# Kernel tuning notes

Hardware: AMD Instinct MI355X
Metric: run time of the kernel (lower is better)

## Reference

```python
import jax, jax.numpy as jnp
import numpy as np

EPS = 1e-6
NUM_HEADS = 16

def layernorm(x, alpha, bias):
    # Faithful to the torch module: torch.std uses ddof=1, and eps is added to std.
    mean = jnp.mean(x, axis=-1, keepdims=True)
    std = jnp.std(x, axis=-1, keepdims=True, ddof=1)
    return alpha * (x - mean) / (std + EPS) + bias

def setup_inputs() -> dict:
    key = jax.random.key(0)
    B, S, D, F = 4, 2048, 1024, 4096
    ks = jax.random.split(key, 8)
    s = 1.0 / np.sqrt(D)
    inp = {
        'x': jax.random.normal(ks[0], (B, S, D), jnp.float32),
        'src_mask': jnp.ones((B, 1, 1, S), jnp.int32),
        'wq': jax.random.normal(ks[1], (D, D), jnp.float32) * s,
        'bq': jnp.zeros((D,), jnp.float32),
        'wk': jax.random.normal(ks[2], (D, D), jnp.float32) * s,
        'bk': jnp.zeros((D,), jnp.float32),
        'wv': jax.random.normal(ks[3], (D, D), jnp.float32) * s,
        'bv': jnp.zeros((D,), jnp.float32),
        'wo': jax.random.normal(ks[4], (D, D), jnp.float32) * s,
        'bo': jnp.zeros((D,), jnp.float32),
        'w1': jax.random.normal(ks[5], (D, F), jnp.float32) * s,
        'b1': jnp.zeros((F,), jnp.float32),
        'w2': jax.random.normal(ks[6], (F, D), jnp.float32) * (1.0 / np.sqrt(F)),
        'b2': jnp.zeros((D,), jnp.float32),
        'ln1_a': jnp.ones((D,), jnp.float32),
        'ln1_b': jnp.zeros((D,), jnp.float32),
        'ln2_a': jnp.ones((D,), jnp.float32),
        'ln2_b': jnp.zeros((D,), jnp.float32),
    }
    return inp

def mha(x, src_mask, wq, bq, wk, bk, wv, bv, wo, bo):
    B, S, D = x.shape
    H = NUM_HEADS
    dk = D // H
    q = (x @ wq + bq).reshape(B, S, H, dk).transpose(0, 2, 1, 3)  # [B,H,S,dk]
    k = (x @ wk + bk).reshape(B, S, H, dk).transpose(0, 2, 1, 3)
    v = (x @ wv + bv).reshape(B, S, H, dk).transpose(0, 2, 1, 3)
    scores = jnp.einsum('bhqd,bhkd->bhqk', q, k) / np.sqrt(dk)  # [B,H,S,S]
    scores = jnp.where(src_mask == 0, -1e9, scores)
    p = jax.nn.softmax(scores, axis=-1)
    ctx = jnp.einsum('bhqk,bhkd->bhqd', p, v)  # [B,H,S,dk]
    ctx = ctx.transpose(0, 2, 1, 3).reshape(B, S, D)
    return ctx @ wo + bo

def reference(x, src_mask, wq, bq, wk, bk, wv, bv, wo, bo,
              w1, b1, w2, b2, ln1_a, ln1_b, ln2_a, ln2_b):
    # residual 1: pre-norm self-attention (dropout is identity in eval)
    h = x + mha(layernorm(x, ln1_a, ln1_b), src_mask, wq, bq, wk, bk, wv, bv, wo, bo)
    # residual 2: pre-norm FFN
    hn = layernorm(h, ln2_a, ln2_b)
    ffn = jax.nn.relu(hn @ w1 + b1) @ w2 + b2
    return h + ffn
```

## Files before the change

### kernel.cpp

```cpp
#include <hip/hip_runtime.h>
#include <hip/hip_bf16.h>

typedef __attribute__((ext_vector_type(8))) short bf16x8;
typedef __attribute__((ext_vector_type(4))) float f32x4;
typedef __hip_bfloat16 bf16;
typedef unsigned short u16;

#define B_ 4
#define S_ 2048
#define D_ 1024
#define F_ 4096
#define H_ 16
#define MROWS 8192

__device__ __forceinline__ u16 f2bf_bits(float f){
  union{bf16 h; u16 u;} x; x.h = __float2bfloat16(f); return x.u;
}
__device__ __forceinline__ unsigned packbf(float a, float b){
  return (unsigned)f2bf_bits(a) | ((unsigned)f2bf_bits(b)<<16);
}
__device__ __forceinline__ void gll16(const bf16* gp, u16* lp){
  __builtin_amdgcn_global_load_lds(
      (const __attribute__((address_space(1))) void*)gp,
      (__attribute__((address_space(3))) void*)lp, 16, 0, 0);
}

__global__ __launch_bounds__(256) void transpose_to_bf16(
    const float* __restrict__ W, bf16* __restrict__ WT, int K, int N)
{
  __shared__ float t[32][33];
  int n0 = blockIdx.x*32, k0 = blockIdx.y*32;
  int x = threadIdx.x, y = threadIdx.y;
  #pragma unroll
  for (int i=0;i<32;i+=8)
    t[y+i][x] = W[(size_t)(k0+y+i)*N + n0+x];
  __syncthreads();
  #pragma unroll
  for (int i=0;i<32;i+=8)
    WT[(size_t)(n0+y+i)*K + k0+x] = __float2bfloat16(t[x][y+i]);
}

__global__ __launch_bounds__(256) void concat_bias(
    const float* __restrict__ bq, const float* __restrict__ bk,
    const float* __restrict__ bv, float* __restrict__ out)
{
  int i = blockIdx.x*256 + threadIdx.x;
  float v = (i < 1024) ? bq[i] : (i < 2048) ? bk[i-1024] : bv[i-2048];
  out[i] = v;
}

__global__ __launch_bounds__(256) void v_transpose(
    const bf16* __restrict__ qkv, bf16* __restrict__ vT)
{
  __shared__ u16 tile[64*65];
  const int bh = blockIdx.y, b = bh>>4, h = bh&15;
  const int s0 = blockIdx.x*64;
  const int tid = threadIdx.x;
  const bf16* src = qkv + (size_t)(b*S_ + s0)*3072 + 2048 + h*64;
  #pragma unroll
  for (int i=0;i<2;i++){
    int idx = i*256 + tid;
    int r = idx>>3, sg = idx&7;
    uint4 v = *reinterpret_cast<const uint4*>(src + (size_t)r*3072 + sg*8);
    const u16* e = (const u16*)&v;
    #pragma unroll
    for (int j=0;j<8;j++) tile[r*65 + sg*8 + j] = e[j];
  }
  __syncthreads();
  bf16* dst = vT + (size_t)bh*64*S_ + s0;
  #pragma unroll
  for (int i=0;i<2;i++){
    int idx = i*256 + tid;
    int d = idx>>3, sg = idx&7;
    u16 tmp[8];
    #pragma unroll
    for (int j=0;j<8;j++) tmp[j] = tile[(sg*8+j)*65 + d];
    *reinterpret_cast<uint4*>(dst + (size_t)d*S_ + sg*8) = *reinterpret_cast<uint4*>(tmp);
  }
}

__device__ __forceinline__ float block_reduce_256(float v, float* sbuf){
  #pragma unroll
  for (int o=32;o>0;o>>=1) v += __shfl_down(v, o);
  int wave = threadIdx.x>>6;
  if ((threadIdx.x&63)==0) sbuf[wave] = v;
  __syncthreads();
  float r = sbuf[0]+sbuf[1]+sbuf[2]+sbuf[3];
  __syncthreads();
  return r;
}

__global__ __launch_bounds__(256) void ln_fwd(
    const float* __restrict__ x, const float* __restrict__ alpha,
    const float* __restrict__ beta, bf16* __restrict__ out)
{
  __shared__ float sbuf[4];
  int row = blockIdx.x, tid = threadIdx.x;
  const float4* xr = reinterpret_cast<const float4*>(x + (size_t)row*D_);
  float4 v = xr[tid];
  float sum = block_reduce_256(v.x+v.y+v.z+v.w, sbuf);
  float mean = sum * (1.0f/1024.0f);
  float dx0=v.x-mean, dx1=v.y-mean, dx2=v.z-mean, dx3=v.w-mean;
  float ssq = block_reduce_256(dx0*dx0+dx1*dx1+dx2*dx2+dx3*dx3, sbuf);
  float std_ = sqrtf(ssq * (1.0f/1023.0f));
  float inv = 1.0f/(std_ + 1e-6f);
  const float4* ar = reinterpret_cast<const float4*>(alpha);
  const float4* br = reinterpret_cast<const float4*>(beta);
  float4 a = ar[tid], bb = br[tid];
  unsigned* o = reinterpret_cast<unsigned*>(out + (size_t)row*D_);
  o[tid*2+0] = packbf(a.x*dx0*inv + bb.x, a.y*dx1*inv + bb.y);
  o[tid*2+1] = packbf(a.z*dx2*inv + bb.z, a.w*dx3*inv + bb.w);
}

template<int EPI>
__global__ __launch_bounds__(256) void gemm_bt(
    const bf16* __restrict__ A, const bf16* __restrict__ BT,
    const float* __restrict__ bias, const float* __restrict__ res,
    void* __restrict__ out, int M, int N, int K)
{
  __shared__ __align__(16) u16 As[128*32];
  __shared__ __align__(16) u16 Bs[128*32];
  const int tid = threadIdx.x;
  const int m0 = blockIdx.x*128, n0 = blockIdx.y*128;
  const int wave = tid>>6, lane = tid&63;
  const int wm = (wave>>1)*64, wn = (wave&1)*64;
  const int lrow = lane&15, quad = lane>>4;
  const int srow = wave*32 + (lane>>2);
  const int sseg = lane&3;
  const bf16* apg = A  + (size_t)(m0+srow)*K + sseg*8;
  const bf16* bpg = BT + (size_t)(n0+srow)*K + sseg*8;
  u16* asd = &As[wave*1024];
  u16* bsd = &Bs[wave*1024];

  f32x4 acc[4][4];
  #pragma unroll
  for (int i=0;i<4;i++)
    #pragma unroll
    for (int j=0;j<4;j++) acc[i][j] = (f32x4){0.f,0.f,0.f,0.f};

  for (int k0=0; k0<K; k0+=32) {
    gll16(apg + k0,                 asd);
    gll16(apg + k0 + (size_t)16*K,  asd + 512);
    gll16(bpg + k0,                 bsd);
    gll16(bpg + k0 + (size_t)16*K,  bsd + 512);
    __syncthreads();
    bf16x8 a[4], b[4];
    #pragma unroll
    for (int t=0;t<4;t++){
      a[t] = *reinterpret_cast<const bf16x8*>(&As[(wm + t*16 + lrow)*32 + quad*8]);
      b[t] = *reinterpret_cast<const bf16x8*>(&Bs[(wn + t*16 + lrow)*32 + quad*8]);
    }
    #pragma unroll
    for (int mt=0;mt<4;mt++)
      #pragma unroll
      for (int nt=0;nt<4;nt++)
        acc[mt][nt] = __builtin_amdgcn_mfma_f32_16x16x32_bf16(a[mt], b[nt], acc[mt][nt], 0,0,0);
    __syncthreads();
  }

  #pragma unroll
  for (int mt=0;mt<4;mt++){
    #pragma unroll
    for (int nt=0;nt<4;nt++){
      int col = n0 + wn + nt*16 + lrow;
      float bv = bias[col];
      #pragma unroll
      for (int r=0;r<4;r++){
        int row = m0 + wm + mt*16 + quad*4 + r;
        size_t idx = (size_t)row*N + col;
        float val = acc[mt][nt][r] + bv;
        if (EPI == 1) val = fmaxf(val, 0.0f);
        if (EPI == 2) {
          ((float*)out)[idx] = val + res[idx];
        } else {
          ((bf16*)out)[idx] = __float2bfloat16(val);
        }
      }
    }
  }
}

#define KP 72

__global__ __launch_bounds__(256) void flash_attn_mfma(
    const bf16* __restrict__ qkv, const bf16* __restrict__ vT,
    const int* __restrict__ mask, bf16* __restrict__ ctx)
{
  __shared__ __align__(16) u16 Ks[64*KP];
  __shared__ __align__(16) u16 Vt[64*KP];
  __shared__ __align__(16) u16 Ps[4][32*KP];
  __shared__ float Mb[64];

  const int b = blockIdx.z, h = blockIdx.y, qt = blockIdx.x;
  const int tid = threadIdx.x, wave = tid>>6, lane = tid&63;
  const int lr = lane&15, quad = lane>>4;
  const int qbase = qt*128 + wave*32;

  const bf16* base = qkv + (size_t)b*S_*3072 + h*64;
  const bf16* vtb  = vT + (size_t)(b*H_+h)*64*S_;
  const int*  mrow = mask + b*S_;

  bf16x8 qf[2][2];
  #pragma unroll
  for (int c=0;c<2;c++){
    const bf16* qp = base + (size_t)(qbase + c*16 + lr)*3072 + quad*8;
    qf[c][0] = *reinterpret_cast<const bf16x8*>(qp);
    qf[c][1] = *reinterpret_cast<const bf16x8*>(qp + 32);
  }

  f32x4 actx[2][4];
  #pragma unroll
  for (int c=0;c<2;c++)
    #pragma unroll
    for (int dt=0;dt<4;dt++) actx[c][dt] = (f32x4){0.f,0.f,0.f,0.f};
  float lsum[2][4] = {{0.f,0.f,0.f,0.f},{0.f,0.f,0.f,0.f}};

  u16* pw = &Ps[wave][0];

  for (int kt=0; kt<S_; kt+=64){
    #pragma unroll
    for (int i=0;i<2;i++){
      int idx = i*256 + tid;
      int r = idx>>3, sg = idx&7;
      *reinterpret_cast<uint4*>(&Ks[r*KP + sg*8]) =
        *reinterpret_cast<const uint4*>(base + 1024 + (size_t)(kt+r)*3072 + sg*8);
      *reinterpret_cast<uint4*>(&Vt[r*KP + sg*8]) =
        *reinterpret_cast<const uint4*>(vtb + (size_t)r*S_ + kt + sg*8);
    }
    if (tid < 64) Mb[tid] = (mrow[kt+tid]==0) ? -1e9f : 0.0f;
    __syncthreads();

    float p[2][4][4];
    #pragma unroll
    for (int nt=0;nt<4;nt++){
      bf16x8 kf0 = *reinterpret_cast<const bf16x8*>(&Ks[(nt*16+lr)*KP + quad*8]);
      bf16x8 kf1 = *reinterpret_cast<const bf16x8*>(&Ks[(nt*16+lr)*KP + 32 + quad*8]);
      float mb = Mb[nt*16+lr];
      #pragma unroll
      for (int c=0;c<2;c++){
        f32x4 a = (f32x4){0.f,0.f,0.f,0.f};
        a = __builtin_amdgcn_mfma_f32_16x16x32_bf16(qf[c][0], kf0, a, 0,0,0);
        a = __builtin_amdgcn_mfma_f32_16x16x32_bf16(qf[c][1], kf1, a, 0,0,0);
        #pragma unroll
        for (int r=0;r<4;r++){
          float e = __expf(a[r]*0.125f + mb);
          p[c][nt][r] = e;
          lsum[c][r] += e;
        }
      }
    }
    #pragma unroll
    for (int c=0;c<2;c++)
      #pragma unroll
      for (int nt=0;nt<4;nt++)
        #pragma unroll
        for (int r=0;r<4;r++)
          pw[(c*16+quad*4+r)*KP + nt*16 + lr] = f2bf_bits(p[c][nt][r]);

    bf16x8 pa[2][2];
    #pragma unroll
    for (int c=0;c<2;c++){
      pa[c][0] = *reinterpret_cast<const bf16x8*>(&pw[(c*16+lr)*KP + quad*8]);
      pa[c][1] = *reinterpret_cast<const bf16x8*>(&pw[(c*16+lr)*KP + 32 + quad*8]);
    }
    #pragma unroll
    for (int dt=0;dt<4;dt++){
      bf16x8 vf0 = *reinterpret_cast<const bf16x8*>(&Vt[(dt*16+lr)*KP + quad*8]);
      bf16x8 vf1 = *reinterpret_cast<const bf16x8*>(&Vt[(dt*16+lr)*KP + 32 + quad*8]);
      #pragma unroll
      for (int c=0;c<2;c++){
        actx[c][dt] = __builtin_amdgcn_mfma_f32_16x16x32_bf16(pa[c][0], vf0, actx[c][dt], 0,0,0);
        actx[c][dt] = __builtin_amdgcn_mfma_f32_16x16x32_bf16(pa[c][1], vf1, actx[c][dt], 0,0,0);
      }
    }
    __syncthreads();
  }

  #pragma unroll
  for (int c=0;c<2;c++)
    #pragma unroll
    for (int r=0;r<4;r++){
      float l = lsum[c][r];
      #pragma unroll
      for (int o=1;o<16;o<<=1) l += __shfl_xor(l, o);
      float inv = 1.0f/l;
      bf16* op = ctx + ((size_t)(b*S_ + qbase + c*16 + quad*4 + r))*D_ + h*64 + lr;
      #pragma unroll
      for (int dt=0;dt<4;dt++)
        op[dt*16] = __float2bfloat16(actx[c][dt][r]*inv);
    }
}

extern "C" void kernel_launch(void* const* d_in, const int* in_sizes, int n_in,
                              void* d_out, int out_size, void* d_ws, size_t ws_size,
                              hipStream_t stream) {
  const float* x    = (const float*)d_in[0];
  const int*   mask = (const int*)  d_in[1];
  const float* wq   = (const float*)d_in[2];
  const float* bq   = (const float*)d_in[3];
  const float* wk   = (const float*)d_in[4];
  const float* bk   = (const float*)d_in[5];
  const float* wv   = (const float*)d_in[6];
  const float* bv   = (const float*)d_in[7];
  const float* wo   = (const float*)d_in[8];
  const float* bo   = (const float*)d_in[9];
  const float* w1   = (const float*)d_in[10];
  const float* b1   = (const float*)d_in[11];
  const float* w2   = (const float*)d_in[12];
  const float* b2   = (const float*)d_in[13];
  const float* ln1a = (const float*)d_in[14];
  const float* ln1b = (const float*)d_in[15];
  const float* ln2a = (const float*)d_in[16];
  const float* ln2b = (const float*)d_in[17];

  char* ws = (char*)d_ws;
  bf16*  wqkvT = (bf16*) (ws + 0);
  bf16*  woT   = (bf16*) (ws + 6291456);
  bf16*  w1T   = (bf16*) (ws + 8388608);
  bf16*  w2T   = (bf16*) (ws + 16777216);
  float* bqkv  = (float*)(ws + 25165824);
  bf16*  xn    = (bf16*) (ws + 25178112);
  bf16*  vT    = (bf16*) (ws + 25178112);
  bf16*  qkv   = (bf16*) (ws + 41955328);
  bf16*  ctx   = (bf16*) (ws + 92286976);
  bf16*  hn    = (bf16*) (ws + 109064192);
  bf16*  act   = (bf16*) (ws + 25178112);

  dim3 tb(32,8);
  transpose_to_bf16<<<dim3(32,32), tb,0,stream>>>(wq, wqkvT,               1024,1024);
  transpose_to_bf16<<<dim3(32,32), tb,0,stream>>>(wk, wqkvT + 1024*1024,   1024,1024);
  transpose_to_bf16<<<dim3(32,32), tb,0,stream>>>(wv, wqkvT + 2*1024*1024, 1024,1024);
  transpose_to_bf16<<<dim3(32,32), tb,0,stream>>>(wo, woT,                 1024,1024);
  transpose_to_bf16<<<dim3(128,32),tb,0,stream>>>(w1, w1T,                 1024,4096);
  transpose_to_bf16<<<dim3(32,128),tb,0,stream>>>(w2, w2T,                 4096,1024);
  concat_bias<<<12,256,0,stream>>>(bq,bk,bv,bqkv);

  ln_fwd<<<8192,256,0,stream>>>(x, ln1a, ln1b, xn);
  gemm_bt<0><<<dim3(64,24),256,0,stream>>>(xn, wqkvT, bqkv, nullptr, qkv, MROWS,3072,1024);
  v_transpose<<<dim3(32,64),256,0,stream>>>(qkv, vT);
  flash_attn_mfma<<<dim3(S_/128,H_,B_),256,0,stream>>>(qkv, vT, mask, ctx);
  gemm_bt<2><<<dim3(64,8),256,0,stream>>>(ctx, woT, bo, x, d_out, MROWS,1024,1024);
  ln_fwd<<<8192,256,0,stream>>>((const float*)d_out, ln2a, ln2b, hn);
  gemm_bt<1><<<dim3(64,32),256,0,stream>>>(hn, w1T, b1, nullptr, act, MROWS,F_,1024);
  gemm_bt<2><<<dim3(64,8),256,0,stream>>>(act, w2T, b2, (const float*)d_out, d_out, MROWS,1024,F_);
}
```

Before: 607.9 us.

## Keep attention probabilities in registers via transposed MFMA and double queries per wave

The attention kernel now computes S^T (K as the A operand), so each lane's exp outputs already sit in the B-operand layout of a 16x16x16 bf16 MFMA for P·V. This removes the LDS round-trip for P, the per-wave Ps buffer and its writes and reads. Each wave now handles 64 query rows instead of 32, so each K/V tile is reused across twice as many queries, and the grid is halved. It also switches to exp2 with a folded scale, vectorized mask reads and packed output stores. The cost is higher register pressure from the larger accumulators and fewer blocks in flight.

```diff
diff --git a/kernel.cpp b/kernel.cpp
--- a/kernel.cpp
+++ b/kernel.cpp
@@ -2,6 +2,7 @@
 #include <hip/hip_bf16.h>
 
 typedef __attribute__((ext_vector_type(8))) short bf16x8;
+typedef __attribute__((ext_vector_type(4))) short bf16x4;
 typedef __attribute__((ext_vector_type(4))) float f32x4;
 typedef __hip_bfloat16 bf16;
 typedef unsigned short u16;
@@ -188,34 +189,31 @@
 {
   __shared__ __align__(16) u16 Ks[64*KP];
   __shared__ __align__(16) u16 Vt[64*KP];
-  __shared__ __align__(16) u16 Ps[4][32*KP];
-  __shared__ float Mb[64];
+  __shared__ __align__(16) float Mb[64];
 
   const int b = blockIdx.z, h = blockIdx.y, qt = blockIdx.x;
   const int tid = threadIdx.x, wave = tid>>6, lane = tid&63;
   const int lr = lane&15, quad = lane>>4;
-  const int qbase = qt*128 + wave*32;
+  const int qbase = qt*256 + wave*64;
 
   const bf16* base = qkv + (size_t)b*S_*3072 + h*64;
   const bf16* vtb  = vT + (size_t)(b*H_+h)*64*S_;
   const int*  mrow = mask + b*S_;
 
-  bf16x8 qf[2][2];
-  #pragma unroll
-  for (int c=0;c<2;c++){
+  bf16x8 qf[4][2];
+  #pragma unroll
+  for (int c=0;c<4;c++){
     const bf16* qp = base + (size_t)(qbase + c*16 + lr)*3072 + quad*8;
     qf[c][0] = *reinterpret_cast<const bf16x8*>(qp);
     qf[c][1] = *reinterpret_cast<const bf16x8*>(qp + 32);
   }
 
-  f32x4 actx[2][4];
-  #pragma unroll
-  for (int c=0;c<2;c++)
+  f32x4 actx[4][4];
+  #pragma unroll
+  for (int c=0;c<4;c++)
     #pragma unroll
     for (int dt=0;dt<4;dt++) actx[c][dt] = (f32x4){0.f,0.f,0.f,0.f};
-  float lsum[2][4] = {{0.f,0.f,0.f,0.f},{0.f,0.f,0.f,0.f}};
-
-  u16* pw = &Ps[wave][0];
+  float lsum[4] = {0.f,0.f,0.f,0.f};
 
   for (int kt=0; kt<S_; kt+=64){
     #pragma unroll
@@ -227,68 +225,62 @@
       *reinterpret_cast<uint4*>(&Vt[r*KP + sg*8]) =
         *reinterpret_cast<const uint4*>(vtb + (size_t)r*S_ + kt + sg*8);
     }
-    if (tid < 64) Mb[tid] = (mrow[kt+tid]==0) ? -1e9f : 0.0f;
+    if (tid < 64) Mb[tid] = (mrow[kt+tid]==0) ? -2e9f : 0.0f;
     __syncthreads();
 
-    float p[2][4][4];
+    bf16x4 pk[4][4];
     #pragma unroll
     for (int nt=0;nt<4;nt++){
       bf16x8 kf0 = *reinterpret_cast<const bf16x8*>(&Ks[(nt*16+lr)*KP + quad*8]);
       bf16x8 kf1 = *reinterpret_cast<const bf16x8*>(&Ks[(nt*16+lr)*KP + 32 + quad*8]);
-      float mb = Mb[nt*16+lr];
+      float4 mb = *reinterpret_cast<const float4*>(&Mb[nt*16 + quad*4]);
+      float mbv[4] = {mb.x, mb.y, mb.z, mb.w};
       #pragma unroll
-      for (int c=0;c<2;c++){
+      for (int c=0;c<4;c++){
         f32x4 a = (f32x4){0.f,0.f,0.f,0.f};
-        a = __builtin_amdgcn_mfma_f32_16x16x32_bf16(qf[c][0], kf0, a, 0,0,0);
-        a = __builtin_amdgcn_mfma_f32_16x16x32_bf16(qf[c][1], kf1, a, 0,0,0);
+        a = __builtin_amdgcn_mfma_f32_16x16x32_bf16(kf0, qf[c][0], a, 0,0,0);
+        a = __builtin_amdgcn_mfma_f32_16x16x32_bf16(kf1, qf[c][1], a, 0,0,0);
+        u16 eb[4];
         #pragma unroll
         for (int r=0;r<4;r++){
-          float e = __expf(a[r]*0.125f + mb);
-          p[c][nt][r] = e;
-          lsum[c][r] += e;
+          float e = exp2f(fmaf(a[r], 0.18033688011116012f, mbv[r]));
+          lsum[c] += e;
+          eb[r] = f2bf_bits(e);
         }
+        bf16x4 t; t[0]=(short)eb[0]; t[1]=(short)eb[1]; t[2]=(short)eb[2]; t[3]=(short)eb[3];
+        pk[c][nt] = t;
       }
     }
-    #pragma unroll
-    for (int c=0;c<2;c++)
+
+    #pragma unroll
+    for (int dt=0;dt<4;dt++){
       #pragma unroll
-      for (int nt=0;nt<4;nt++)
+      for (int kc=0;kc<4;kc++){
+        bf16x4 vf = *reinterpret_cast<const bf16x4*>(&Vt[(dt*16+lr)*KP + kc*16 + quad*4]);
         #pragma unroll
-        for (int r=0;r<4;r++)
-          pw[(c*16+quad*4+r)*KP + nt*16 + lr] = f2bf_bits(p[c][nt][r]);
-
-    bf16x8 pa[2][2];
-    #pragma unroll
-    for (int c=0;c<2;c++){
-      pa[c][0] = *reinterpret_cast<const bf16x8*>(&pw[(c*16+lr)*KP + quad*8]);
-      pa[c][1] = *reinterpret_cast<const bf16x8*>(&pw[(c*16+lr)*KP + 32 + quad*8]);
-    }
+        for (int c=0;c<4;c++)
+          actx[c][dt] = __builtin_amdgcn_mfma_f32_16x16x16bf16_1k(vf, pk[c][kc], actx[c][dt], 0,0,0);
+      }
+    }
+    __syncthreads();
+  }
+
+  #pragma unroll
+  for (int c=0;c<4;c++){
+    float l = lsum[c];
+    l += __shfl_xor(l, 16);
+    l += __shfl_xor(l, 32);
+    float inv = 1.0f/l;
+    int q = qbase + c*16 + lr;
+    bf16* op = ctx + (size_t)(b*S_+q)*D_ + h*64 + quad*4;
     #pragma unroll
     for (int dt=0;dt<4;dt++){
-      bf16x8 vf0 = *reinterpret_cast<const bf16x8*>(&Vt[(dt*16+lr)*KP + quad*8]);
-      bf16x8 vf1 = *reinterpret_cast<const bf16x8*>(&Vt[(dt*16+lr)*KP + 32 + quad*8]);
-      #pragma unroll
-      for (int c=0;c<2;c++){
-        actx[c][dt] = __builtin_amdgcn_mfma_f32_16x16x32_bf16(pa[c][0], vf0, actx[c][dt], 0,0,0);
-        actx[c][dt] = __builtin_amdgcn_mfma_f32_16x16x32_bf16(pa[c][1], vf1, actx[c][dt], 0,0,0);
-      }
-    }
-    __syncthreads();
-  }
-
-  #pragma unroll
-  for (int c=0;c<2;c++)
-    #pragma unroll
-    for (int r=0;r<4;r++){
-      float l = lsum[c][r];
-      #pragma unroll
-      for (int o=1;o<16;o<<=1) l += __shfl_xor(l, o);
-      float inv = 1.0f/l;
-      bf16* op = ctx + ((size_t)(b*S_ + qbase + c*16 + quad*4 + r))*D_ + h*64 + lr;
-      #pragma unroll
-      for (int dt=0;dt<4;dt++)
-        op[dt*16] = __float2bfloat16(actx[c][dt][r]*inv);
-    }
+      uint2 o;
+      o.x = packbf(actx[c][dt][0]*inv, actx[c][dt][1]*inv);
+      o.y = packbf(actx[c][dt][2]*inv, actx[c][dt][3]*inv);
+      *reinterpret_cast<uint2*>(op + dt*16) = o;
+    }
+  }
 }
 
 extern "C" void kernel_launch(void* const* d_in, const int* in_sizes, int n_in,
@@ -338,7 +330,7 @@
   ln_fwd<<<8192,256,0,stream>>>(x, ln1a, ln1b, xn);
   gemm_bt<0><<<dim3(64,24),256,0,stream>>>(xn, wqkvT, bqkv, nullptr, qkv, MROWS,3072,1024);
   v_transpose<<<dim3(32,64),256,0,stream>>>(qkv, vT);
-  flash_attn_mfma<<<dim3(S_/128,H_,B_),256,0,stream>>>(qkv, vT, mask, ctx);
+  flash_attn_mfma<<<dim3(S_/256,H_,B_),256,0,stream>>>(qkv, vT, mask, ctx);
   gemm_bt<2><<<dim3(64,8),256,0,stream>>>(ctx, woT, bo, x, d_out, MROWS,1024,1024);
   ln_fwd<<<8192,256,0,stream>>>((const float*)d_out, ln2a, ln2b, hn);
   gemm_bt<1><<<dim3(64,32),256,0,stream>>>(hn, w1T, b1, nullptr, act, MROWS,F_,1024);
```

After: 612.5 us. No clear change (+0.8%).
